# Performance work log

Measured on AMD Instinct MI355X. Metric: run time of the kernel, lower is better.

## Reference

```python
import jax, jax.numpy as jnp
import numpy as np

C, H, W = 3, 2048, 2048
N_BOXES = 256
HEIGHT = 32  # target_height


def _make_boxes():
    # Realistic text-line quads: TL, TR, BR, BL corners.
    rng = np.random.RandomState(0)
    x0 = rng.uniform(0, W - 500, N_BOXES)
    y0 = rng.uniform(0, H - 60, N_BOXES)
    bw = rng.uniform(100, 400, N_BOXES)
    bh = rng.uniform(20, 40, N_BOXES)
    p0 = np.stack([x0, y0], -1)
    p1 = np.stack([x0 + bw, y0], -1)
    p2 = np.stack([x0 + bw, y0 + bh], -1)
    p3 = np.stack([x0, y0 + bh], -1)
    return np.stack([p0, p1, p2, p3], 1).astype(np.float32)  # [N,4,2]


def setup_inputs() -> dict:
    key = jax.random.key(0)
    img = jax.random.normal(key, (C, H, W), dtype=jnp.float32)
    boxes = jnp.asarray(_make_boxes())
    scale = jnp.ones((1,), dtype=jnp.float32)
    return {"img": img, "boxes": boxes, "scale": scale}


def reference(img, boxes, scale):
    height = HEIGHT
    boxes = boxes / scale  # [N,4,2]
    img_c, img_h, img_w = img.shape

    h_dists = jnp.linalg.norm(boxes[:, 2] - boxes[:, 1], axis=1)
    w_dists = jnp.linalg.norm(boxes[:, 1] - boxes[:, 0], axis=1)
    # torch .long() truncates toward zero; values are positive here.
    widths = (height * w_dists / jnp.clip(h_dists, 1e-6)).astype(jnp.int32)
    max_w = int(widths.max()) // 8 * 8 + 8  # concrete (data-dependent shape)

    rows = jnp.arange(height, dtype=jnp.float32) / (height - 1)
    cols = jnp.arange(max_w, dtype=jnp.float32)
    y = rows[None, :, None]        # broadcasts to [N,height,max_w]
    x_idx = cols[None, None, :]
    curr_w = widths.astype(jnp.float32)[:, None, None]
    x = x_idx / jnp.clip(curr_w - 1.0, 1.0)

    def _interp(idx):
        v0 = boxes[:, 0, idx][:, None, None]
        v1 = boxes[:, 1, idx][:, None, None]
        v2 = boxes[:, 2, idx][:, None, None]
        v3 = boxes[:, 3, idx][:, None, None]
        return (1 - x) * (1 - y) * v0 + x * (1 - y) * v1 + x * y * v2 + (1 - x) * y * v3

    res_x = _interp(0)  # [N,height,max_w]
    res_y = _interp(1)
    mask = x_idx < curr_w
    grid_c = jnp.where(mask, res_x / (img_w - 1.0) * 2.0 - 1.0, 2.0)
    grid_r = jnp.where(mask, res_y / (img_h - 1.0) * 2.0 - 1.0, 2.0)

    # grid_sample(mode='nearest', padding_mode='zeros', align_corners=True)
    ix = jnp.round((grid_c + 1.0) * (img_w - 1) * 0.5)
    iy = jnp.round((grid_r + 1.0) * (img_h - 1) * 0.5)
    inb = (ix >= 0) & (ix <= img_w - 1) & (iy >= 0) & (iy <= img_h - 1)
    ixc = jnp.clip(ix, 0, img_w - 1).astype(jnp.int32)
    iyc = jnp.clip(iy, 0, img_h - 1).astype(jnp.int32)
    samp = img[:, iyc, ixc]                    # [C,N,height,max_w]
    out = jnp.where(inb[None], samp, 0.0).transpose(1, 0, 2, 3)  # [N,C,height,max_w]

    widths_out = (widths // 8 * 8 + 8).astype(jnp.int32)
    return out, widths_out
```

## Files before the change

### kernel.cpp

```cpp
#include <hip/hip_runtime.h>

constexpr int kC = 3;
constexpr int kH = 2048;
constexpr int kW = 2048;
constexpr int kNB = 256;
constexpr int kHeight = 32;

typedef float f32x4 __attribute__((ext_vector_type(4)));

__global__ __launch_bounds__(256) void boxprep_kernel(
    const float* __restrict__ boxes,
    const float* __restrict__ scale,
    float* __restrict__ params,
    float* __restrict__ out_tail)
{
    const int b = threadIdx.x;
    const float s = scale[0];
    const float* bx = boxes + b * 8;
    float p[8];
#pragma unroll
    for (int k = 0; k < 8; ++k) p[k] = bx[k] / s;

    const float hdx = p[4] - p[2], hdy = p[5] - p[3];
    const float h_dist = sqrtf(hdx * hdx + hdy * hdy);
    const float wdx = p[2] - p[0], wdy = p[3] - p[1];
    const float w_dist = sqrtf(wdx * wdx + wdy * wdy);
    const int width = (int)(32.0f * w_dist / fmaxf(h_dist, 1e-6f));
    const float curr_w = (float)width;
    const float inv_xden = 1.0f / fmaxf(curr_w - 1.0f, 1.0f);

    float* pp = params + b * 16;
#pragma unroll
    for (int k = 0; k < 8; ++k) pp[k] = p[k];
    pp[8] = curr_w;
    pp[9] = inv_xden;

    out_tail[b] = (float)(width / 8 * 8 + 8);
}

__global__ __launch_bounds__(64) void extract_kernel(
    const float* __restrict__ img,
    const float* __restrict__ params,
    float* __restrict__ out,
    int max_w)
{
    const int r = blockIdx.y;
    const int b = blockIdx.z;
    const int c0 = (blockIdx.x * 64 + threadIdx.x) * 4;
    if (c0 >= max_w) return;

    const float* pp = params + b * 16;
    const float p0x = pp[0], p0y = pp[1];
    const float p1x = pp[2], p1y = pp[3];
    const float p2x = pp[4], p2y = pp[5];
    const float p3x = pp[6], p3y = pp[7];
    const float curr_w = pp[8];
    const float inv_xden = pp[9];

    const size_t ch_stride = (size_t)kHeight * max_w;
    const size_t obase = (((size_t)b * kC) * (size_t)kHeight + (size_t)r) * (size_t)max_w + (size_t)c0;

    f32x4 o0 = {0.f, 0.f, 0.f, 0.f};
    f32x4 o1 = {0.f, 0.f, 0.f, 0.f};
    f32x4 o2 = {0.f, 0.f, 0.f, 0.f};

    if ((float)c0 < curr_w) {
        const float y = (float)r / 31.0f;
        const float omy = 1.0f - y;
        constexpr float invW1 = 1.0f / 2047.0f;
#pragma unroll
        for (int j = 0; j < 4; ++j) {
            const float cf = (float)(c0 + j);
            if (cf < curr_w) {
                const float x = cf * inv_xden;
                const float omx = 1.0f - x;
                const float w00 = omx * omy;
                const float w10 = x * omy;
                const float w11 = x * y;
                const float w01 = omx * y;
                const float res_x = w00 * p0x + w10 * p1x + w11 * p2x + w01 * p3x;
                const float res_y = w00 * p0y + w10 * p1y + w11 * p2y + w01 * p3y;

                const float grid_c = res_x * invW1 * 2.0f - 1.0f;
                const float grid_r = res_y * invW1 * 2.0f - 1.0f;
                const float fix = rintf((grid_c + 1.0f) * 2047.0f * 0.5f);
                const float fiy = rintf((grid_r + 1.0f) * 2047.0f * 0.5f);
                const bool inb = (fix >= 0.0f) && (fix <= 2047.0f) &&
                                 (fiy >= 0.0f) && (fiy <= 2047.0f);
                const int ixc = (int)fminf(fmaxf(fix, 0.0f), 2047.0f);
                const int iyc = (int)fminf(fmaxf(fiy, 0.0f), 2047.0f);

                const size_t ipix = (size_t)iyc * kW + (size_t)ixc;
                const float v0 = img[ipix];
                const float v1 = img[(size_t)kH * kW + ipix];
                const float v2 = img[2 * (size_t)kH * kW + ipix];
                o0[j] = inb ? v0 : 0.0f;
                o1[j] = inb ? v1 : 0.0f;
                o2[j] = inb ? v2 : 0.0f;
            }
        }
    }

    *(f32x4*)(out + obase) = o0;
    *(f32x4*)(out + obase + ch_stride) = o1;
    *(f32x4*)(out + obase + 2 * ch_stride) = o2;
}

extern "C" void kernel_launch(void* const* d_in, const int* in_sizes, int n_in,
                              void* d_out, int out_size, void* d_ws, size_t ws_size,
                              hipStream_t stream) {
    const float* img   = (const float*)d_in[0];
    const float* boxes = (const float*)d_in[1];
    const float* scale = (const float*)d_in[2];
    float* out = (float*)d_out;
    float* params = (float*)d_ws;

    const int max_w = (out_size - kNB) / (kNB * kC * kHeight);
    const int quads = max_w / 4;

    boxprep_kernel<<<1, kNB, 0, stream>>>(boxes, scale, params,
                                          out + (size_t)kNB * kC * kHeight * max_w);

    dim3 grid((quads + 63) / 64, kHeight, kNB);
    extract_kernel<<<grid, dim3(64, 1, 1), 0, stream>>>(img, params, out, max_w);
}
```

Before: 24.76 us.

## Stage box row window into LDS with coalesced loads before nearest sampling

Each block now handles one output row of one box and first loads a contiguous window of the source image row (per channel) into shared memory with vectorized coalesced loads. Per-pixel samples that land on the staged row and window are read from LDS; anything else falls back to the global gather. The launch geometry changes from 64-thread blocks per column chunk to 256-thread blocks per (row, box), which adds a barrier and staging of up to 416 floats per channel, some of which may be unused.

Result: no change. 24.48 us (-1.1%).

```diff
diff --git a/kernel.cpp b/kernel.cpp
--- a/kernel.cpp
+++ b/kernel.cpp
@@ -5,6 +5,7 @@
 constexpr int kW = 2048;
 constexpr int kNB = 256;
 constexpr int kHeight = 32;
+constexpr int kWin = 416;
 
 typedef float f32x4 __attribute__((ext_vector_type(4)));
 
@@ -29,26 +30,40 @@
     const float curr_w = (float)width;
     const float inv_xden = 1.0f / fmaxf(curr_w - 1.0f, 1.0f);
 
+    const float xlo = fminf(p[0], p[6]);
+    const float xhi = fmaxf(p[2], p[4]);
+    int wbase = (int)floorf(xlo) - 2;
+    if (wbase < 0) wbase = 0;
+    wbase &= ~3;
+    int wend = (int)ceilf(xhi) + 2;
+    if (wend > kW - 1) wend = kW - 1;
+    int wlen = wend - wbase + 1;
+    wlen = (wlen + 3) & ~3;
+    if (wbase + wlen > kW) wlen = kW - wbase;
+    if (wlen > kWin) wlen = kWin;
+    if (wlen < 4) wlen = 4;
+
     float* pp = params + b * 16;
 #pragma unroll
     for (int k = 0; k < 8; ++k) pp[k] = p[k];
-    pp[8] = curr_w;
-    pp[9] = inv_xden;
+    pp[8]  = curr_w;
+    pp[9]  = inv_xden;
+    pp[10] = __int_as_float(wbase);
+    pp[11] = __int_as_float(wlen);
 
     out_tail[b] = (float)(width / 8 * 8 + 8);
 }
 
-__global__ __launch_bounds__(64) void extract_kernel(
+__global__ __launch_bounds__(256) void extract_kernel(
     const float* __restrict__ img,
     const float* __restrict__ params,
     float* __restrict__ out,
     int max_w)
 {
-    const int r = blockIdx.y;
-    const int b = blockIdx.z;
-    const int c0 = (blockIdx.x * 64 + threadIdx.x) * 4;
-    if (c0 >= max_w) return;
+    __shared__ float lds[3][kWin];
 
+    const int r = blockIdx.x;
+    const int b = blockIdx.y;
     const float* pp = params + b * 16;
     const float p0x = pp[0], p0y = pp[1];
     const float p1x = pp[2], p1y = pp[3];
@@ -56,54 +71,87 @@
     const float p3x = pp[6], p3y = pp[7];
     const float curr_w = pp[8];
     const float inv_xden = pp[9];
+    const int wbase = __float_as_int(pp[10]);
+    const int wlen  = __float_as_int(pp[11]);
+
+    const float y = (float)r / 31.0f;
+    const float omy = 1.0f - y;
+    constexpr float invW1 = 1.0f / 2047.0f;
+
+    {
+    }
+    const float x0_ = 0.0f * inv_xden;
+    const float omx0_ = 1.0f - x0_;
+    const float w00_ = omx0_ * omy, w10_ = x0_ * omy, w11_ = x0_ * y, w01_ = omx0_ * y;
+    const float ry0 = ((w00_ * p0y + w10_ * p1y) + w11_ * p2y) + w01_ * p3y;
+    const float gr0 = ry0 * invW1 * 2.0f - 1.0f;
+    const float fiy0 = rintf((gr0 + 1.0f) * 2047.0f * 0.5f);
+    const bool stage_ok = (fiy0 >= 0.0f) && (fiy0 <= 2047.0f);
+    const int iy0 = (int)fminf(fmaxf(fiy0, 0.0f), 2047.0f);
+
+    const int nq_win = wlen >> 2;
+#pragma unroll
+    for (int ch = 0; ch < 3; ++ch) {
+        const float* src = img + (size_t)ch * kH * kW + (size_t)iy0 * kW + wbase;
+        for (int t4 = threadIdx.x; t4 < nq_win; t4 += 256) {
+            *(f32x4*)&lds[ch][t4 * 4] = *(const f32x4*)&src[t4 * 4];
+        }
+    }
+    __syncthreads();
 
     const size_t ch_stride = (size_t)kHeight * max_w;
-    const size_t obase = (((size_t)b * kC) * (size_t)kHeight + (size_t)r) * (size_t)max_w + (size_t)c0;
+    const size_t rowbase = ((size_t)b * (kC * kHeight) + (size_t)r) * (size_t)max_w;
+    const float wlo = (float)wbase;
+    const float whi = (float)(wbase + wlen);
 
-    f32x4 o0 = {0.f, 0.f, 0.f, 0.f};
-    f32x4 o1 = {0.f, 0.f, 0.f, 0.f};
-    f32x4 o2 = {0.f, 0.f, 0.f, 0.f};
+    const int nq = max_w >> 2;
+    for (int qi = threadIdx.x; qi < nq; qi += 256) {
+        const int c0 = qi * 4;
+        f32x4 o0 = {0.f, 0.f, 0.f, 0.f};
+        f32x4 o1 = {0.f, 0.f, 0.f, 0.f};
+        f32x4 o2 = {0.f, 0.f, 0.f, 0.f};
 
-    if ((float)c0 < curr_w) {
-        const float y = (float)r / 31.0f;
-        const float omy = 1.0f - y;
-        constexpr float invW1 = 1.0f / 2047.0f;
+        if ((float)c0 < curr_w) {
 #pragma unroll
-        for (int j = 0; j < 4; ++j) {
-            const float cf = (float)(c0 + j);
-            if (cf < curr_w) {
-                const float x = cf * inv_xden;
-                const float omx = 1.0f - x;
-                const float w00 = omx * omy;
-                const float w10 = x * omy;
-                const float w11 = x * y;
-                const float w01 = omx * y;
-                const float res_x = w00 * p0x + w10 * p1x + w11 * p2x + w01 * p3x;
-                const float res_y = w00 * p0y + w10 * p1y + w11 * p2y + w01 * p3y;
+            for (int j = 0; j < 4; ++j) {
+                const float cf = (float)(c0 + j);
+                if (cf < curr_w) {
+                    const float x = cf * inv_xden;
+                    const float omx = 1.0f - x;
+                    const float w00 = omx * omy;
+                    const float w10 = x * omy;
+                    const float w11 = x * y;
+                    const float w01 = omx * y;
+                    const float res_x = ((w00 * p0x + w10 * p1x) + w11 * p2x) + w01 * p3x;
+                    const float res_y = ((w00 * p0y + w10 * p1y) + w11 * p2y) + w01 * p3y;
+                    const float grid_c = res_x * invW1 * 2.0f - 1.0f;
+                    const float grid_r = res_y * invW1 * 2.0f - 1.0f;
+                    const float fix = rintf((grid_c + 1.0f) * 2047.0f * 0.5f);
+                    const float fiy = rintf((grid_r + 1.0f) * 2047.0f * 0.5f);
 
-                const float grid_c = res_x * invW1 * 2.0f - 1.0f;
-                const float grid_r = res_y * invW1 * 2.0f - 1.0f;
-                const float fix = rintf((grid_c + 1.0f) * 2047.0f * 0.5f);
-                const float fiy = rintf((grid_r + 1.0f) * 2047.0f * 0.5f);
-                const bool inb = (fix >= 0.0f) && (fix <= 2047.0f) &&
-                                 (fiy >= 0.0f) && (fiy <= 2047.0f);
-                const int ixc = (int)fminf(fmaxf(fix, 0.0f), 2047.0f);
-                const int iyc = (int)fminf(fmaxf(fiy, 0.0f), 2047.0f);
-
-                const size_t ipix = (size_t)iyc * kW + (size_t)ixc;
-                const float v0 = img[ipix];
-                const float v1 = img[(size_t)kH * kW + ipix];
-                const float v2 = img[2 * (size_t)kH * kW + ipix];
-                o0[j] = inb ? v0 : 0.0f;
-                o1[j] = inb ? v1 : 0.0f;
-                o2[j] = inb ? v2 : 0.0f;
+                    if (stage_ok && fiy == fiy0 && fix >= wlo && fix < whi) {
+                        const int t = (int)fix - wbase;
+                        o0[j] = lds[0][t];
+                        o1[j] = lds[1][t];
+                        o2[j] = lds[2][t];
+                    } else {
+                        const bool inb = (fix >= 0.0f) && (fix <= 2047.0f) &&
+                                         (fiy >= 0.0f) && (fiy <= 2047.0f);
+                        const int ixc = (int)fminf(fmaxf(fix, 0.0f), 2047.0f);
+                        const int iyc = (int)fminf(fmaxf(fiy, 0.0f), 2047.0f);
+                        const size_t ipix = (size_t)iyc * kW + (size_t)ixc;
+                        o0[j] = inb ? img[ipix] : 0.0f;
+                        o1[j] = inb ? img[(size_t)kH * kW + ipix] : 0.0f;
+                        o2[j] = inb ? img[2 * (size_t)kH * kW + ipix] : 0.0f;
+                    }
+                }
             }
         }
+
+        *(f32x4*)(out + rowbase + c0) = o0;
+        *(f32x4*)(out + rowbase + ch_stride + c0) = o1;
+        *(f32x4*)(out + rowbase + 2 * ch_stride + c0) = o2;
     }
-
-    *(f32x4*)(out + obase) = o0;
-    *(f32x4*)(out + obase + ch_stride) = o1;
-    *(f32x4*)(out + obase + 2 * ch_stride) = o2;
 }
 
 extern "C" void kernel_launch(void* const* d_in, const int* in_sizes, int n_in,
@@ -116,11 +164,10 @@
     float* params = (float*)d_ws;
 
     const int max_w = (out_size - kNB) / (kNB * kC * kHeight);
-    const int quads = max_w / 4;
 
     boxprep_kernel<<<1, kNB, 0, stream>>>(boxes, scale, params,
                                           out + (size_t)kNB * kC * kHeight * max_w);
 
-    dim3 grid((quads + 63) / 64, kHeight, kNB);
-    extract_kernel<<<grid, dim3(64, 1, 1), 0, stream>>>(img, params, out, max_w);
+    dim3 grid(kHeight, kNB);
+    extract_kernel<<<grid, dim3(256, 1, 1), 0, stream>>>(img, params, out, max_w);
 }
```
